# Kernel tuning notes

Measured on AMD Instinct MI355X. Metric: run time of the kernel, lower is better.

## Reference

```python
import jax, jax.numpy as jnp
import numpy as np

B, N, D, H, DK, DI = 64, 256, 1024, 8, 64, 2048
NEG = -1e9
SCALE = 1.0 / np.sqrt(DK).astype(np.float32)


def _ln(x, s, b, eps=1e-5):
    m = jnp.mean(x, axis=-1, keepdims=True)
    v = jnp.var(x, axis=-1, keepdims=True)
    return (x - m) * jax.lax.rsqrt(v + eps) * s + b


def _glat_basic(x, mask, npm, wq, wk, wv, wo, bo, ls1, lb1, w1, b1, w2, b2, ls2, lb2):
    # mask: [B,1,N,N] bool, True = blocked
    b, n, d = x.shape
    q = (x @ wq).reshape(b, n, H, DK).transpose(0, 2, 1, 3)  # [B,H,N,DK]
    k = (x @ wk).reshape(b, n, H, DK).transpose(0, 2, 1, 3)
    v = (x @ wv).reshape(b, n, H, DK).transpose(0, 2, 1, 3)
    scores = jnp.einsum('bhqd,bhkd->bhqk', q, k) * SCALE
    scores = jnp.where(mask, NEG, scores)
    attn = jax.nn.softmax(scores, axis=-1)
    out = jnp.einsum('bhqk,bhkd->bhqd', attn, v)
    out = out.transpose(0, 2, 1, 3).reshape(b, n, H * DK)
    out = out @ wo + bo
    out = _ln(out + x, ls1, lb1)           # attn residual + layernorm
    out = out * npm                         # non_pad_mask
    h = jax.nn.relu(out @ w1 + b1) @ w2 + b2
    out2 = _ln(h + out, ls2, lb2) * npm     # FFN residual + layernorm + mask
    return out2


def setup_inputs():
    key = jax.random.key(0)
    ks = jax.random.split(key, 40)
    p = lambda i, shape: jax.random.normal(ks[i], shape, jnp.float32) * 0.02
    inp = {
        'x': jax.random.normal(ks[0], (B, N, D), jnp.float32),
        'adj': jax.random.randint(ks[1], (B, N, N), 0, 2).astype(jnp.int32),
        'non_pad_mask': jnp.ones((B, N, 1), jnp.float32),
        'slf_attn_mask': jnp.zeros((B, N, N), jnp.int32),
    }
    i = 2
    for t in ('g', 'l'):
        inp[f'wq_{t}'] = p(i, (D, H * DK)); i += 1
        inp[f'wk_{t}'] = p(i, (D, H * DK)); i += 1
        inp[f'wv_{t}'] = p(i, (D, H * DK)); i += 1
        inp[f'wo_{t}'] = p(i, (H * DK, D)); i += 1
        inp[f'bo_{t}'] = jnp.zeros((D,), jnp.float32)
        inp[f'ln1s_{t}'] = jnp.ones((D,), jnp.float32)
        inp[f'ln1b_{t}'] = jnp.zeros((D,), jnp.float32)
        inp[f'w1_{t}'] = p(i, (D, DI)); i += 1
        inp[f'b1_{t}'] = jnp.zeros((DI,), jnp.float32)
        inp[f'w2_{t}'] = p(i, (DI, D)); i += 1
        inp[f'b2_{t}'] = jnp.zeros((D,), jnp.float32)
        inp[f'ln2s_{t}'] = jnp.ones((D,), jnp.float32)
        inp[f'ln2b_{t}'] = jnp.zeros((D,), jnp.float32)
    inp['fc_w'] = p(i, (2 * D, D)); i += 1
    inp['fc_b'] = jnp.zeros((D,), jnp.float32)
    return inp


def reference(x, adj, non_pad_mask, slf_attn_mask,
              wq_g, wk_g, wv_g, wo_g, bo_g, ln1s_g, ln1b_g, w1_g, b1_g, w2_g, b2_g, ln2s_g, ln2b_g,
              wq_l, wk_l, wv_l, wo_l, bo_l, ln1s_l, ln1b_l, w1_l, b1_l, w2_l, b2_l, ln2s_l, ln2b_l,
              fc_w, fc_b):
    pad_mask = (slf_attn_mask[:, None, :, :] != 0)            # [B,1,N,N]
    local_mask = pad_mask | (adj[:, None, :, :] == 0)         # local: only attend along edges
    x_g = _glat_basic(x, pad_mask, non_pad_mask,
                      wq_g, wk_g, wv_g, wo_g, bo_g, ln1s_g, ln1b_g,
                      w1_g, b1_g, w2_g, b2_g, ln2s_g, ln2b_g)
    x_l = _glat_basic(x, local_mask, non_pad_mask,
                      wq_l, wk_l, wv_l, wo_l, bo_l, ln1s_l, ln1b_l,
                      w1_l, b1_l, w2_l, b2_l, ln2s_l, ln2b_l)
    out = jnp.concatenate([x_g, x_l], axis=-1) @ fc_w + fc_b
    return out
```

## Files before the change

### kernel.cpp

```cpp
#include <hip/hip_runtime.h>


typedef unsigned short u16;
typedef unsigned long long u64;
typedef __bf16 bf16_t;
typedef bf16_t bf16x8 __attribute__((ext_vector_type(8)));
typedef float  f32x4  __attribute__((ext_vector_type(4)));
typedef u16    u16x8  __attribute__((ext_vector_type(8)));
typedef u16    u16x4  __attribute__((ext_vector_type(4)));

__device__ __forceinline__ float bf2f(u16 u){
  union { unsigned int i; float f; } c; c.i = ((unsigned int)u) << 16; return c.f;
}
__device__ __forceinline__ u16 f2bf(float f){
  union { float f; unsigned int u; } c; c.f = f;
  unsigned int u = c.u;
  unsigned int r = (u + 0x7fffu + ((u >> 16) & 1u)) >> 16;
  return (u16)r;
}

__device__ __forceinline__ void gl16(const u16* g, u16* l){
  __builtin_amdgcn_global_load_lds(
      (const __attribute__((address_space(1))) void*)g,
      (__attribute__((address_space(3))) void*)l, 16, 0, 0);
}

__global__ __launch_bounds__(256) void zero_out(float* out, int n){
  for (int i = blockIdx.x * 256 + threadIdx.x; i < n; i += 256 * 4096) out[i] = 0.f;
}

__global__ __launch_bounds__(256) void cvt_bf16(
    const float* __restrict__ in, u16* __restrict__ out)
{
  const size_t i = ((size_t)blockIdx.x * 256 + threadIdx.x) * 8;
  f32x4 a = *(const f32x4*)&in[i];
  f32x4 b = *(const f32x4*)&in[i + 4];
  u16x8 o;
  #pragma unroll
  for (int j = 0; j < 4; ++j){ o[j] = f2bf(a[j]); o[4+j] = f2bf(b[j]); }
  *(u16x8*)&out[i] = o;
}

__global__ __launch_bounds__(256) void transpose_w(
    const float* __restrict__ src, u16* __restrict__ dst, int K, int N, int dstOff)
{
  __shared__ u16 tile[32][33];
  const int bk = blockIdx.x * 32, bn = blockIdx.y * 32;
  const int t = threadIdx.x;
  const int r = t >> 5, c = t & 31;
  #pragma unroll
  for (int p = 0; p < 4; ++p)
    tile[r + p*8][c] = f2bf(src[(size_t)(bk + r + p*8) * N + bn + c]);
  __syncthreads();
  #pragma unroll
  for (int p = 0; p < 4; ++p)
    dst[(size_t)(dstOff + bn + r + p*8) * K + bk + c] = tile[c][r + p*8];
}

__global__ __launch_bounds__(256) void transpose_w3(
    const float* __restrict__ sA, const float* __restrict__ sB,
    const float* __restrict__ sC, u16* __restrict__ dst, int K, int N)
{
  __shared__ u16 tile[32][33];
  const float* src = blockIdx.z == 0 ? sA : (blockIdx.z == 1 ? sB : sC);
  const int dstOff = blockIdx.z * N;
  const int bk = blockIdx.x * 32, bn = blockIdx.y * 32;
  const int t = threadIdx.x;
  const int r = t >> 5, c = t & 31;
  #pragma unroll
  for (int p = 0; p < 4; ++p)
    tile[r + p*8][c] = f2bf(src[(size_t)(bk + r + p*8) * N + bn + c]);
  __syncthreads();
  #pragma unroll
  for (int p = 0; p < 4; ++p)
    dst[(size_t)(dstOff + bn + r + p*8) * K + bk + c] = tile[c][r + p*8];
}

template<int RELU, int OF32, int ACC>
__global__ __launch_bounds__(512, 2) void gemm256(
    const u16* __restrict__ A0, const u16* __restrict__ A1,
    int Astride, int ksplit,
    const u16* __restrict__ BT, int Bld, int M, int N, int K,
    const float* __restrict__ bias, void* __restrict__ outv, int out_ld)
{
  __shared__ u16 lds[2*32768];
  const int tid  = threadIdx.x;
  const int lane = tid & 63;
  const int wid  = tid >> 6;
  const int wm = wid >> 2, wn = wid & 3;
  const int l15 = lane & 15, l4 = lane >> 4;
  const int m0 = blockIdx.x * 256, n0 = blockIdx.y * 256;

  f32x4 acc[8][4];
  #pragma unroll
  for (int i = 0; i < 8; ++i)
    #pragma unroll
    for (int j = 0; j < 4; ++j)
      acc[i][j] = (f32x4){0.f, 0.f, 0.f, 0.f};

  const int s0 = tid, s1 = tid + 512;
  const int r0 = s0 >> 3, g0 = (s0 & 7) ^ (r0 & 7);
  const int r1 = s1 >> 3, g1 = (s1 & 7) ^ (r1 & 7);

  const int nt = K >> 6;

  auto stageA = [&](int kt, int h, int buf){
    const int kb = kt * 64;
    const u16* Ab = A0; int kl = kb;
    if (kb >= ksplit){ Ab = A1; kl = kb - ksplit; }
    u16* dst = &lds[buf*32768 + h*8192];
    gl16(&Ab[(size_t)(m0 + h*128 + r0) * Astride + kl + g0*8], &dst[s0*8]);
    gl16(&Ab[(size_t)(m0 + h*128 + r1) * Astride + kl + g1*8], &dst[s1*8]);
  };
  auto stageB = [&](int kt, int h, int buf){
    const int kb = kt * 64;
    u16* dst = &lds[buf*32768 + 16384 + h*8192];
    gl16(&BT[(size_t)(n0 + h*128 + r0) * Bld + kb + g0*8], &dst[s0*8]);
    gl16(&BT[(size_t)(n0 + h*128 + r1) * Bld + kb + g1*8], &dst[s1*8]);
  };
  auto lda = [&](int i, int kc, int buf) -> bf16x8 {
    const int r = wm*128 + i*16 + l15;
    const int c = (kc*4 + l4) ^ (r & 7);
    return *(const bf16x8*)&lds[buf*32768 + r*64 + c*8];
  };
  auto ldb = [&](int j, int kc, int buf) -> bf16x8 {
    const int r = wn*64 + j*16 + l15;
    const int c = (kc*4 + l4) ^ (r & 7);
    return *(const bf16x8*)&lds[buf*32768 + 16384 + r*64 + c*8];
  };

  stageA(0, 0, 0); stageA(0, 1, 0); stageB(0, 0, 0); stageB(0, 1, 0);

  for (int t = 0; t < nt; ++t){
    const int buf = t & 1, nbuf = buf ^ 1;
    const bool pf = (t + 1 < nt);
    if (pf){
      stageA(t+1, 0, nbuf);
      asm volatile("s_waitcnt vmcnt(2)" ::: "memory");
    } else {
      asm volatile("s_waitcnt vmcnt(0)" ::: "memory");
    }
    __builtin_amdgcn_sched_barrier(0);
    __builtin_amdgcn_s_barrier();
    __builtin_amdgcn_sched_barrier(0);

    bf16x8 a_[4][2], b_[2][2];
    #pragma unroll
    for (int i = 0; i < 4; ++i){ a_[i][0] = lda(i, 0, buf); a_[i][1] = lda(i, 1, buf); }
    #pragma unroll
    for (int j = 0; j < 2; ++j){ b_[j][0] = ldb(j, 0, buf); b_[j][1] = ldb(j, 1, buf); }
    if (pf) stageA(t+1, 1, nbuf);
    __builtin_amdgcn_s_setprio(1);
    #pragma unroll
    for (int i = 0; i < 4; ++i)
      #pragma unroll
      for (int j = 0; j < 2; ++j){
        acc[i][j] = __builtin_amdgcn_mfma_f32_16x16x32_bf16(a_[i][0], b_[j][0], acc[i][j], 0,0,0);
        acc[i][j] = __builtin_amdgcn_mfma_f32_16x16x32_bf16(a_[i][1], b_[j][1], acc[i][j], 0,0,0);
      }
    __builtin_amdgcn_s_setprio(0);
    #pragma unroll
    for (int j = 0; j < 2; ++j){ b_[j][0] = ldb(2+j, 0, buf); b_[j][1] = ldb(2+j, 1, buf); }
    if (pf) stageB(t+1, 0, nbuf);
    __builtin_amdgcn_s_setprio(1);
    #pragma unroll
    for (int i = 0; i < 4; ++i)
      #pragma unroll
      for (int j = 0; j < 2; ++j){
        acc[i][2+j] = __builtin_amdgcn_mfma_f32_16x16x32_bf16(a_[i][0], b_[j][0], acc[i][2+j], 0,0,0);
        acc[i][2+j] = __builtin_amdgcn_mfma_f32_16x16x32_bf16(a_[i][1], b_[j][1], acc[i][2+j], 0,0,0);
      }
    __builtin_amdgcn_s_setprio(0);
    #pragma unroll
    for (int i = 0; i < 4; ++i){ a_[i][0] = lda(4+i, 0, buf); a_[i][1] = lda(4+i, 1, buf); }
    if (pf) stageB(t+1, 1, nbuf);
    __builtin_amdgcn_s_setprio(1);
    #pragma unroll
    for (int i = 0; i < 4; ++i)
      #pragma unroll
      for (int j = 0; j < 2; ++j){
        acc[4+i][2+j] = __builtin_amdgcn_mfma_f32_16x16x32_bf16(a_[i][0], b_[j][0], acc[4+i][2+j], 0,0,0);
        acc[4+i][2+j] = __builtin_amdgcn_mfma_f32_16x16x32_bf16(a_[i][1], b_[j][1], acc[4+i][2+j], 0,0,0);
      }
    __builtin_amdgcn_s_setprio(0);
    #pragma unroll
    for (int j = 0; j < 2; ++j){ b_[j][0] = ldb(j, 0, buf); b_[j][1] = ldb(j, 1, buf); }
    __builtin_amdgcn_s_setprio(1);
    #pragma unroll
    for (int i = 0; i < 4; ++i)
      #pragma unroll
      for (int j = 0; j < 2; ++j){
        acc[4+i][j] = __builtin_amdgcn_mfma_f32_16x16x32_bf16(a_[i][0], b_[j][0], acc[4+i][j], 0,0,0);
        acc[4+i][j] = __builtin_amdgcn_mfma_f32_16x16x32_bf16(a_[i][1], b_[j][1], acc[4+i][j], 0,0,0);
      }
    __builtin_amdgcn_s_setprio(0);

    __builtin_amdgcn_sched_barrier(0);
    __builtin_amdgcn_s_barrier();
    __builtin_amdgcn_sched_barrier(0);
  }

  const int rb = m0 + wm*128 + l4*4;
  const int cb = n0 + wn*64 + l15;
  #pragma unroll
  for (int i = 0; i < 8; ++i){
    #pragma unroll
    for (int j = 0; j < 4; ++j){
      const int col = cb + j*16;
      const float badd = bias ? bias[col] : 0.f;
      #pragma unroll
      for (int r = 0; r < 4; ++r){
        const int row = rb + i*16 + r;
        float y = acc[i][j][r] + badd;
        if (RELU) y = y > 0.f ? y : 0.f;
        if (OF32){
          float* po = &((float*)outv)[(size_t)row * out_ld + col];
          if (ACC) y += *po;
          *po = y;
        } else {
          u16* po = &((u16*)outv)[(size_t)row * out_ld + col];
          if (ACC) y += bf2f(*po);
          *po = f2bf(y);
        }
      }
    }
  }
}

__global__ __launch_bounds__(256) void mask_pack(
    const int* __restrict__ slf, const int* __restrict__ adj,
    u64* __restrict__ mb_g, u64* __restrict__ mb_l)
{
  const int idx  = blockIdx.x * 4 + (threadIdx.x >> 6);
  const int lane = threadIdx.x & 63;
  const size_t mi = (size_t)(idx >> 2) * 256 + (size_t)(idx & 3) * 64 + lane;
  const bool g = slf[mi] != 0;
  const bool l = g || (adj[mi] == 0);
  const u64 bg = __ballot(g);
  const u64 bl = __ballot(l);
  if (lane == 0){ mb_g[idx] = bg; mb_l[idx] = bl; }
}

__global__ __launch_bounds__(256) void attn_mfma(
    const u16* __restrict__ qkv, const u64* __restrict__ mb,
    int boff, u16* __restrict__ out)
{
  __shared__ u16 kbuf[64*64];
  __shared__ u16 vtbuf[64*64];
  __shared__ u16 pbuf[4][32*64];

  const int b_loc = blockIdx.x >> 4;
  const int h     = (blockIdx.x >> 1) & 7;
  const int qt    = blockIdx.x & 1;
  const int b     = boff + b_loc;
  const int t     = threadIdx.x;
  const int w     = t >> 6, lane = t & 63;
  const int l15   = lane & 15, l4 = lane >> 4;

  bf16x8 qf[2][2];
  {
    const int rbase = b_loc*256 + qt*128 + w*32;
    #pragma unroll
    for (int i = 0; i < 2; ++i)
      #pragma unroll
      for (int kc = 0; kc < 2; ++kc)
        qf[i][kc] = *(const bf16x8*)&qkv[(size_t)(rbase + i*16 + l15)*1536 + h*64 + kc*32 + l4*8];
  }

  f32x4 acc_o[2][4];
  float m_[2][4], l_[2][4];
  #pragma unroll
  for (int i = 0; i < 2; ++i){
    #pragma unroll
    for (int j = 0; j < 4; ++j) acc_o[i][j] = (f32x4){0.f,0.f,0.f,0.f};
    #pragma unroll
    for (int r = 0; r < 4; ++r){ m_[i][r] = -1e30f; l_[i][r] = 0.f; }
  }

  for (int c = 0; c < 4; ++c){
    __syncthreads();
    {
      const int kr = t >> 2, dg = (t & 3) * 16;
      const size_t rbase = (size_t)(b_loc*256 + c*64 + kr)*1536 + h*64 + dg;
      u16x8 k0 = *(const u16x8*)&qkv[rbase + 512];
      u16x8 k1 = *(const u16x8*)&qkv[rbase + 512 + 8];
      u16x8 v0 = *(const u16x8*)&qkv[rbase + 1024];
      u16x8 v1 = *(const u16x8*)&qkv[rbase + 1024 + 8];
      const int sw = (kr & 7) << 3;
      *(u16x8*)&kbuf[kr*64 + (dg ^ sw)]       = k0;
      *(u16x8*)&kbuf[kr*64 + ((dg + 8) ^ sw)] = k1;
      #pragma unroll
      for (int e = 0; e < 8; ++e){
        const int d0 = dg + e, d1 = dg + 8 + e;
        vtbuf[d0*64 + (kr ^ ((d0 & 7) << 3))] = v0[e];
        vtbuf[d1*64 + (kr ^ ((d1 & 7) << 3))] = v1[e];
      }
    }
    __syncthreads();

    bf16x8 kfr[4][2];
    #pragma unroll
    for (int jb = 0; jb < 4; ++jb){
      const int key = jb*16 + l15;
      const int sw = (key & 7) << 3;
      #pragma unroll
      for (int kc = 0; kc < 2; ++kc)
        kfr[jb][kc] = *(const bf16x8*)&kbuf[key*64 + ((kc*32 + l4*8) ^ sw)];
    }
    f32x4 s_[2][4];
    #pragma unroll
    for (int i = 0; i < 2; ++i)
      #pragma unroll
      for (int jb = 0; jb < 4; ++jb){
        f32x4 a = (f32x4){0.f,0.f,0.f,0.f};
        a = __builtin_amdgcn_mfma_f32_16x16x32_bf16(qf[i][0], kfr[jb][0], a, 0,0,0);
        a = __builtin_amdgcn_mfma_f32_16x16x32_bf16(qf[i][1], kfr[jb][1], a, 0,0,0);
        s_[i][jb] = a;
      }

    #pragma unroll
    for (int i = 0; i < 2; ++i)
      #pragma unroll
      for (int r = 0; r < 4; ++r){
        const int qrow = qt*128 + w*32 + i*16 + l4*4 + r;
        const u64 bits = mb[((size_t)b*256 + qrow)*4 + c];
        #pragma unroll
        for (int jb = 0; jb < 4; ++jb){
          float xv = s_[i][jb][r] * 0.125f;
          if ((bits >> (jb*16 + l15)) & 1ull) xv = -1e9f;
          s_[i][jb][r] = xv;
        }
      }
    float mxs[2][4];
    bool okall = true;
    #pragma unroll
    for (int i = 0; i < 2; ++i)
      #pragma unroll
      for (int r = 0; r < 4; ++r){
        float mx = fmaxf(fmaxf(s_[i][0][r], s_[i][1][r]),
                         fmaxf(s_[i][2][r], s_[i][3][r]));
        #pragma unroll
        for (int d = 1; d < 16; d <<= 1)
          mx = fmaxf(mx, __shfl_xor(mx, d, 64));
        mxs[i][r] = mx;
        okall = okall && (mx <= m_[i][r] + 8.f);
      }
    if (__all(okall)){
      #pragma unroll
      for (int i = 0; i < 2; ++i)
        #pragma unroll
        for (int r = 0; r < 4; ++r){
          const int prow = i*16 + l4*4 + r;
          const int swp = (prow & 7) << 3;
          float ps = 0.f;
          #pragma unroll
          for (int jb = 0; jb < 4; ++jb){
            const float p = __expf(s_[i][jb][r] - m_[i][r]);
            ps += p;
            pbuf[w][prow*64 + ((jb*16 + l15) ^ swp)] = f2bf(p);
          }
          #pragma unroll
          for (int d = 1; d < 16; d <<= 1)
            ps += __shfl_xor(ps, d, 64);
          l_[i][r] += ps;
        }
    } else {
      #pragma unroll
      for (int i = 0; i < 2; ++i)
        #pragma unroll
        for (int r = 0; r < 4; ++r){
          const int prow = i*16 + l4*4 + r;
          const float mnew = fmaxf(m_[i][r], mxs[i][r]);
          const float corr = __expf(m_[i][r] - mnew);
          m_[i][r] = mnew;
          float ps = 0.f;
          const int swp = (prow & 7) << 3;
          #pragma unroll
          for (int jb = 0; jb < 4; ++jb){
            const float p = __expf(s_[i][jb][r] - mnew);
            ps += p;
            pbuf[w][prow*64 + ((jb*16 + l15) ^ swp)] = f2bf(p);
          }
          #pragma unroll
          for (int d = 1; d < 16; d <<= 1)
            ps += __shfl_xor(ps, d, 64);
          l_[i][r] = l_[i][r] * corr + ps;
          #pragma unroll
          for (int j2 = 0; j2 < 4; ++j2) acc_o[i][j2][r] *= corr;
        }
    }

    bf16x8 vfr[4][2];
    #pragma unroll
    for (int j2 = 0; j2 < 4; ++j2){
      const int dim = j2*16 + l15;
      const int sw = (dim & 7) << 3;
      #pragma unroll
      for (int kc = 0; kc < 2; ++kc)
        vfr[j2][kc] = *(const bf16x8*)&vtbuf[dim*64 + ((kc*32 + l4*8) ^ sw)];
    }
    #pragma unroll
    for (int i = 0; i < 2; ++i){
      const int prow = i*16 + l15;
      const int swp = (prow & 7) << 3;
      bf16x8 pa0 = *(const bf16x8*)&pbuf[w][prow*64 + ((l4*8) ^ swp)];
      bf16x8 pa1 = *(const bf16x8*)&pbuf[w][prow*64 + ((32 + l4*8) ^ swp)];
      #pragma unroll
      for (int j2 = 0; j2 < 4; ++j2){
        acc_o[i][j2] = __builtin_amdgcn_mfma_f32_16x16x32_bf16(pa0, vfr[j2][0], acc_o[i][j2], 0,0,0);
        acc_o[i][j2] = __builtin_amdgcn_mfma_f32_16x16x32_bf16(pa1, vfr[j2][1], acc_o[i][j2], 0,0,0);
      }
    }
  }

  #pragma unroll
  for (int i = 0; i < 2; ++i){
    #pragma unroll
    for (int r = 0; r < 4; ++r){
      const int qrow = qt*128 + w*32 + i*16 + l4*4 + r;
      const float inv = 1.f / l_[i][r];
      const size_t ob = ((size_t)b*256 + qrow)*512 + h*64;
      #pragma unroll
      for (int j2 = 0; j2 < 4; ++j2)
        out[ob + j2*16 + l15] = f2bf(acc_o[i][j2][r] * inv);
    }
  }
}

template<int RF32>
__global__ __launch_bounds__(256) void ln_fused(
    const u16* a, const void* __restrict__ res,
    const float* __restrict__ sc, const float* __restrict__ bs,
    const float* __restrict__ npm, u16* out)
{
  const int w = threadIdx.x >> 6, lane = threadIdx.x & 63;
  const int row = blockIdx.x * 4 + w;
  const size_t bse = (size_t)row * 1024 + lane * 16;

  u16x8 av0 = *(const u16x8*)&a[bse];
  u16x8 av1 = *(const u16x8*)&a[bse + 8];
  float rv[16];
  if (RF32){
    const float* rp = (const float*)res + bse;
    #pragma unroll
    for (int j = 0; j < 16; j += 4){
      f32x4 q = *(const f32x4*)&rp[j];
      rv[j] = q[0]; rv[j+1] = q[1]; rv[j+2] = q[2]; rv[j+3] = q[3];
    }
  } else {
    const u16* rp = (const u16*)res + bse;
    u16x8 q0 = *(const u16x8*)rp;
    u16x8 q1 = *(const u16x8*)(rp + 8);
    #pragma unroll
    for (int j = 0; j < 8; ++j){ rv[j] = bf2f(q0[j]); rv[8+j] = bf2f(q1[j]); }
  }

  float vv[16]; float s = 0.f, sq = 0.f;
  #pragma unroll
  for (int j = 0; j < 8; ++j){
    vv[j]   = bf2f(av0[j]) + rv[j];
    vv[8+j] = bf2f(av1[j]) + rv[8+j];
  }
  #pragma unroll
  for (int j = 0; j < 16; ++j){ s += vv[j]; sq += vv[j]*vv[j]; }
  #pragma unroll
  for (int i = 1; i < 64; i <<= 1){
    s  += __shfl_xor(s,  i, 64);
    sq += __shfl_xor(sq, i, 64);
  }
  const float mean = s * (1.f/1024.f);
  const float var  = sq * (1.f/1024.f) - mean*mean;
  const float rstd = rsqrtf(var + 1e-5f);
  const float nm   = npm[row];

  u16x8 o0, o1;
  #pragma unroll
  for (int j = 0; j < 8; ++j){
    const int c0 = lane*16 + j, c1 = c0 + 8;
    o0[j] = f2bf(((vv[j]   - mean) * rstd * sc[c0] + bs[c0]) * nm);
    o1[j] = f2bf(((vv[8+j] - mean) * rstd * sc[c1] + bs[c1]) * nm);
  }
  *(u16x8*)&out[bse]     = o0;
  *(u16x8*)&out[bse + 8] = o1;
}

extern "C" void kernel_launch(void* const* d_in, const int* in_sizes, int n_in,
                              void* d_out, int out_size, void* d_ws, size_t ws_size,
                              hipStream_t stream)
{
  const size_t NEED = 58720256ull * 2ull;
  if (ws_size < NEED){
    zero_out<<<4096, 256, 0, stream>>>((float*)d_out, out_size);
    return;
  }

  const float* x   = (const float*)d_in[0];
  const int*   adj = (const int*)d_in[1];
  const float* npm = (const float*)d_in[2];
  const int*   slf = (const int*)d_in[3];
  const float* fcw = (const float*)d_in[30];
  const float* fcb = (const float*)d_in[31];

  u16* ws    = (u16*)d_ws;
  u16* wqkvT = ws;
  u16* woT   = ws + 1572864;
  u16* w1T   = ws + 2097152;
  u16* w2T   = ws + 4194304;
  u16* fcT   = ws + 6291456;
  u16* xbf   = ws + 8388608;
  u16* tmp0  = ws + 8388608;
  u16* qkvh  = ws + 25165824;
  u16* ln1   = ws + 25165824;
  u16* tmp1  = ws + 41943040;

  u16* dout16 = (u16*)d_out;
  u16* attnb0 = dout16;
  u16* attnb1 = dout16 + 8388608;
  u16* hbuf   = dout16;
  u64* mb_g   = (u64*)(dout16 + 16777216);
  u64* mb_l   = mb_g + 65536;

  cvt_bf16<<<8192, 256, 0, stream>>>(x, xbf);
  mask_pack<<<16384, 256, 0, stream>>>(slf, adj, mb_g, mb_l);
  transpose_w<<<dim3(64, 32), 256, 0, stream>>>(fcw, fcT, 2048, 1024, 0);

  for (int L = 0; L < 2; ++L){
    const int bi = 4 + L*13;
    transpose_w3<<<dim3(32, 16, 3), 256, 0, stream>>>(
        (const float*)d_in[bi+0], (const float*)d_in[bi+1],
        (const float*)d_in[bi+2], wqkvT, 1024, 512);
    u16* attnb = L ? attnb1 : attnb0;
    for (int hf = 0; hf < 2; ++hf){
      const u16* xh = xbf + (size_t)hf*8192*1024;
      gemm256<0,0,0><<<dim3(32, 6), 512, 0, stream>>>(
          xh, xh, 1024, 1024, wqkvT, 1024, 8192, 1536, 1024, nullptr, qkvh, 1536);
      attn_mfma<<<512, 256, 0, stream>>>(qkvh, L ? mb_l : mb_g, hf*32, attnb);
    }
  }

  transpose_w<<<dim3(16, 32), 256, 0, stream>>>((const float*)d_in[4+3], woT, 512, 1024, 0);
  gemm256<0,0,0><<<dim3(64, 4), 512, 0, stream>>>(
      attnb0, attnb0, 512, 512, woT, 512, 16384, 1024, 512,
      (const float*)d_in[4+4], tmp0, 1024);
  transpose_w<<<dim3(16, 32), 256, 0, stream>>>((const float*)d_in[17+3], woT, 512, 1024, 0);
  gemm256<0,0,0><<<dim3(64, 4), 512, 0, stream>>>(
      attnb1, attnb1, 512, 512, woT, 512, 16384, 1024, 512,
      (const float*)d_in[17+4], tmp1, 1024);

  for (int L = 0; L < 2; ++L){
    const int bi = 4 + L*13;
    const float* l1s = (const float*)d_in[bi+5];
    const float* l1b = (const float*)d_in[bi+6];
    const float* b1  = (const float*)d_in[bi+8];
    const float* b2  = (const float*)d_in[bi+10];
    const float* l2s = (const float*)d_in[bi+11];
    const float* l2b = (const float*)d_in[bi+12];
    u16* tmpL = L ? tmp1 : tmp0;

    transpose_w<<<dim3(32, 64), 256, 0, stream>>>((const float*)d_in[bi+7], w1T, 1024, 2048, 0);
    transpose_w<<<dim3(64, 32), 256, 0, stream>>>((const float*)d_in[bi+9], w2T, 2048, 1024, 0);

    ln_fused<1><<<4096, 256, 0, stream>>>(tmpL, x, l1s, l1b, npm, ln1);
    gemm256<1,0,0><<<dim3(64, 8), 512, 0, stream>>>(
        ln1, ln1, 1024, 1024, w1T, 1024, 16384, 2048, 1024, b1, hbuf, 2048);
    gemm256<0,0,0><<<dim3(64, 4), 512, 0, stream>>>(
        hbuf, hbuf, 2048, 2048, w2T, 2048, 16384, 1024, 2048, b2, tmpL, 1024);
    ln_fused<0><<<4096, 256, 0, stream>>>(tmpL, ln1, l2s, l2b, npm, tmpL);
  }

  gemm256<0,1,0><<<dim3(64, 4), 512, 0, stream>>>(
      tmp0, tmp1, 1024, 1024, fcT, 2048, 16384, 1024, 2048, fcb, d_out, 1024);
}
```

Baseline: 733.2 us.

## Process full batch per QKV GEMM and batch all weight transposes upfront

Reworks the buffer plan so the QKV projection and attention run over the whole batch of 16384 rows in one launch each, instead of two half-batch passes per layer. The full QKV buffer now lives in the output buffer and the attention outputs move into the workspace. The QKV and Wo weight transposes for both layers are merged into two batched launches at the start. This cuts kernel launches and gives larger grids for better GPU occupancy, at the cost of a bigger QKV intermediate and more workspace aliasing to keep correct.

```diff
diff --git a/kernel.cpp b/kernel.cpp
--- a/kernel.cpp
+++ b/kernel.cpp
@@ -57,13 +57,18 @@
     dst[(size_t)(dstOff + bn + r + p*8) * K + bk + c] = tile[c][r + p*8];
 }
 
-__global__ __launch_bounds__(256) void transpose_w3(
-    const float* __restrict__ sA, const float* __restrict__ sB,
-    const float* __restrict__ sC, u16* __restrict__ dst, int K, int N)
+__global__ __launch_bounds__(256) void transpose_qkv6(
+    const float* s0, const float* s1, const float* s2,
+    const float* s3, const float* s4, const float* s5,
+    u16* __restrict__ dst0, u16* __restrict__ dst1)
 {
   __shared__ u16 tile[32][33];
-  const float* src = blockIdx.z == 0 ? sA : (blockIdx.z == 1 ? sB : sC);
-  const int dstOff = blockIdx.z * N;
+  const int z = blockIdx.z;
+  const float* src = z == 0 ? s0 : z == 1 ? s1 : z == 2 ? s2
+                   : z == 3 ? s3 : z == 4 ? s4 : s5;
+  u16* dst = (z < 3 ? dst0 : dst1);
+  const int dstOff = (z % 3) * 512;
+  const int K = 1024, N = 512;
   const int bk = blockIdx.x * 32, bn = blockIdx.y * 32;
   const int t = threadIdx.x;
   const int r = t >> 5, c = t & 31;
@@ -74,6 +79,25 @@
   #pragma unroll
   for (int p = 0; p < 4; ++p)
     dst[(size_t)(dstOff + bn + r + p*8) * K + bk + c] = tile[c][r + p*8];
+}
+
+__global__ __launch_bounds__(256) void transpose_wo2(
+    const float* s0, const float* s1, u16* __restrict__ dst0, u16* __restrict__ dst1)
+{
+  __shared__ u16 tile[32][33];
+  const float* src = blockIdx.z == 0 ? s0 : s1;
+  u16* dst = blockIdx.z == 0 ? dst0 : dst1;
+  const int K = 512, N = 1024;
+  const int bk = blockIdx.x * 32, bn = blockIdx.y * 32;
+  const int t = threadIdx.x;
+  const int r = t >> 5, c = t & 31;
+  #pragma unroll
+  for (int p = 0; p < 4; ++p)
+    tile[r + p*8][c] = f2bf(src[(size_t)(bk + r + p*8) * N + bn + c]);
+  __syncthreads();
+  #pragma unroll
+  for (int p = 0; p < 4; ++p)
+    dst[(size_t)(bn + r + p*8) * K + bk + c] = tile[c][r + p*8];
 }
 
 template<int RELU, int OF32, int ACC>
@@ -243,23 +267,22 @@
 
 __global__ __launch_bounds__(256) void attn_mfma(
     const u16* __restrict__ qkv, const u64* __restrict__ mb,
-    int boff, u16* __restrict__ out)
+    u16* __restrict__ out)
 {
   __shared__ u16 kbuf[64*64];
   __shared__ u16 vtbuf[64*64];
   __shared__ u16 pbuf[4][32*64];
 
-  const int b_loc = blockIdx.x >> 4;
-  const int h     = (blockIdx.x >> 1) & 7;
-  const int qt    = blockIdx.x & 1;
-  const int b     = boff + b_loc;
-  const int t     = threadIdx.x;
-  const int w     = t >> 6, lane = t & 63;
-  const int l15   = lane & 15, l4 = lane >> 4;
+  const int b  = blockIdx.x >> 4;
+  const int h  = (blockIdx.x >> 1) & 7;
+  const int qt = blockIdx.x & 1;
+  const int t  = threadIdx.x;
+  const int w  = t >> 6, lane = t & 63;
+  const int l15 = lane & 15, l4 = lane >> 4;
 
   bf16x8 qf[2][2];
   {
-    const int rbase = b_loc*256 + qt*128 + w*32;
+    const int rbase = b*256 + qt*128 + w*32;
     #pragma unroll
     for (int i = 0; i < 2; ++i)
       #pragma unroll
@@ -281,7 +304,7 @@
     __syncthreads();
     {
       const int kr = t >> 2, dg = (t & 3) * 16;
-      const size_t rbase = (size_t)(b_loc*256 + c*64 + kr)*1536 + h*64 + dg;
+      const size_t rbase = (size_t)(b*256 + c*64 + kr)*1536 + h*64 + dg;
       u16x8 k0 = *(const u16x8*)&qkv[rbase + 512];
       u16x8 k1 = *(const u16x8*)&qkv[rbase + 512 + 8];
       u16x8 v0 = *(const u16x8*)&qkv[rbase + 1024];
@@ -501,50 +524,50 @@
   const float* fcw = (const float*)d_in[30];
   const float* fcb = (const float*)d_in[31];
 
-  u16* ws    = (u16*)d_ws;
-  u16* wqkvT = ws;
-  u16* woT   = ws + 1572864;
-  u16* w1T   = ws + 2097152;
-  u16* w2T   = ws + 4194304;
-  u16* fcT   = ws + 6291456;
-  u16* xbf   = ws + 8388608;
-  u16* tmp0  = ws + 8388608;
-  u16* qkvh  = ws + 25165824;
-  u16* ln1   = ws + 25165824;
-  u16* tmp1  = ws + 41943040;
+  u16* ws     = (u16*)d_ws;
+  u16* wqkvT0 = ws;
+  u16* wqkvT1 = ws + 1572864;
+  u16* woT0   = ws + 3145728;
+  u16* woT1   = ws + 3670016;
+  u16* fcT    = ws + 4194304;
+  u16* w1T    = ws + 6291456;
+  u16* w2T    = ws;
+  u16* xbf    = ws + 8388608;
+  u16* tmp0   = ws + 8388608;
+  u16* attnb0 = ws + 25165824;
+  u16* attnb1 = ws + 33554432;
+  u16* ln1    = ws + 25165824;
+  u16* tmp1   = ws + 41943040;
 
   u16* dout16 = (u16*)d_out;
-  u16* attnb0 = dout16;
-  u16* attnb1 = dout16 + 8388608;
+  u16* qkv    = dout16;
+  u64* mb_g   = (u64*)(dout16 + 25165824);
+  u64* mb_l   = mb_g + 65536;
   u16* hbuf   = dout16;
-  u64* mb_g   = (u64*)(dout16 + 16777216);
-  u64* mb_l   = mb_g + 65536;
 
   cvt_bf16<<<8192, 256, 0, stream>>>(x, xbf);
   mask_pack<<<16384, 256, 0, stream>>>(slf, adj, mb_g, mb_l);
   transpose_w<<<dim3(64, 32), 256, 0, stream>>>(fcw, fcT, 2048, 1024, 0);
+  transpose_qkv6<<<dim3(32, 16, 6), 256, 0, stream>>>(
+      (const float*)d_in[4+0], (const float*)d_in[4+1], (const float*)d_in[4+2],
+      (const float*)d_in[17+0], (const float*)d_in[17+1], (const float*)d_in[17+2],
+      wqkvT0, wqkvT1);
+  transpose_wo2<<<dim3(16, 32, 2), 256, 0, stream>>>(
+      (const float*)d_in[4+3], (const float*)d_in[17+3], woT0, woT1);
 
   for (int L = 0; L < 2; ++L){
-    const int bi = 4 + L*13;
-    transpose_w3<<<dim3(32, 16, 3), 256, 0, stream>>>(
-        (const float*)d_in[bi+0], (const float*)d_in[bi+1],
-        (const float*)d_in[bi+2], wqkvT, 1024, 512);
+    const u16* wq = L ? wqkvT1 : wqkvT0;
     u16* attnb = L ? attnb1 : attnb0;
-    for (int hf = 0; hf < 2; ++hf){
-      const u16* xh = xbf + (size_t)hf*8192*1024;
-      gemm256<0,0,0><<<dim3(32, 6), 512, 0, stream>>>(
-          xh, xh, 1024, 1024, wqkvT, 1024, 8192, 1536, 1024, nullptr, qkvh, 1536);
-      attn_mfma<<<512, 256, 0, stream>>>(qkvh, L ? mb_l : mb_g, hf*32, attnb);
-    }
-  }
-
-  transpose_w<<<dim3(16, 32), 256, 0, stream>>>((const float*)d_in[4+3], woT, 512, 1024, 0);
+    gemm256<0,0,0><<<dim3(64, 6), 512, 0, stream>>>(
+        xbf, xbf, 1024, 1024, wq, 1024, 16384, 1536, 1024, nullptr, qkv, 1536);
+    attn_mfma<<<1024, 256, 0, stream>>>(qkv, L ? mb_l : mb_g, attnb);
+  }
+
   gemm256<0,0,0><<<dim3(64, 4), 512, 0, stream>>>(
-      attnb0, attnb0, 512, 512, woT, 512, 16384, 1024, 512,
+      attnb0, attnb0, 512, 512, woT0, 512, 16384, 1024, 512,
       (const float*)d_in[4+4], tmp0, 1024);
-  transpose_w<<<dim3(16, 32), 256, 0, stream>>>((const float*)d_in[17+3], woT, 512, 1024, 0);
   gemm256<0,0,0><<<dim3(64, 4), 512, 0, stream>>>(
-      attnb1, attnb1, 512, 512, woT, 512, 16384, 1024, 512,
+      attnb1, attnb1, 512, 512, woT1, 512, 16384, 1024, 512,
       (const float*)d_in[17+4], tmp1, 1024);
 
   for (int L = 0; L < 2; ++L){
```

Result: faster. 713.2 us (-2.7%).
